# Kernel tuning notes

Measured on AMD Instinct MI355X. Metric: run time of the kernel, lower is better.

## Reference

```python
import jax, jax.numpy as jnp
import numpy as np

# Model hyperparameters (Mamba(dim=256, expand=1, d_state=16, bimamba_type='v2'))
D_MODEL = 256      # dim; expand=1 -> d_inner = D_MODEL
D_STATE = 16
DT_RANK = 16       # ceil(256/16)
D_CONV = 4
BATCH = 2
SEQ = 4096         # H*W = 64*64


def _ln(x, g, b, eps=1e-5):
    m = jnp.mean(x, axis=-1, keepdims=True)
    v = jnp.mean((x - m) ** 2, axis=-1, keepdims=True)
    return (x - m) * jax.lax.rsqrt(v + eps) * g + b


def _causal_dwconv(x, w, b):
    # x: [B, L, d], w: [d, 1, K] (depthwise), causal padding K-1 on the left
    xt = jnp.transpose(x, (0, 2, 1))  # [B, d, L]
    y = jax.lax.conv_general_dilated(
        xt, w, window_strides=(1,), padding=[(w.shape[-1] - 1, 0)],
        dimension_numbers=('NCH', 'OIH', 'NCH'), feature_group_count=xt.shape[1])
    return jnp.transpose(y + b[None, :, None], (0, 2, 1))


def _selective_scan(u, dt, Bm, Cm, A, D, z):
    # u, dt, z: [B, L, d]; Bm, Cm: [B, L, N]; A: [d, N]; D: [d]
    def step(h, inp):
        dt_t, B_t, C_t, u_t = inp            # [B,d], [B,N], [B,N], [B,d]
        h = h * jnp.exp(dt_t[:, :, None] * A) + (dt_t * u_t)[:, :, None] * B_t[:, None, :]
        y = jnp.einsum('bdn,bn->bd', h, C_t)
        return h, y

    h0 = jnp.zeros((u.shape[0], u.shape[2], A.shape[1]), u.dtype)
    xs = (jnp.transpose(dt, (1, 0, 2)), jnp.transpose(Bm, (1, 0, 2)),
          jnp.transpose(Cm, (1, 0, 2)), jnp.transpose(u, (1, 0, 2)))
    _, ys = jax.lax.scan(step, h0, xs)       # ys: [L, B, d]
    y = jnp.transpose(ys, (1, 0, 2)) + u * D
    return y * jax.nn.silu(z)                # SiLU(z) gating (done inside mamba_inner_fn)


def _mamba_dir(xin, z, conv_w, conv_b, xproj_w, dtproj_w, dtproj_b, A_log, D):
    u = jax.nn.silu(_causal_dwconv(xin, conv_w, conv_b))
    dbl = u @ xproj_w.T                       # [B, L, dt_rank + 2*N]
    dt = dbl[..., :DT_RANK]
    Bm = dbl[..., DT_RANK:DT_RANK + D_STATE]
    Cm = dbl[..., DT_RANK + D_STATE:]
    dt = jax.nn.softplus(dt @ dtproj_w.T + dtproj_b)
    return _selective_scan(u, dt, Bm, Cm, -jnp.exp(A_log), D, z)


def setup_inputs() -> dict:
    key = jax.random.key(0)
    ks = jax.random.split(key, 24)
    d, N, R, K = D_MODEL, D_STATE, DT_RANK, D_CONV
    s = 0.02
    A_log = jnp.log(jnp.tile(jnp.arange(1, N + 1, dtype=jnp.float32)[None, :], (d, 1)))
    return {
        'input': jax.random.normal(ks[0], (BATCH, SEQ, d), jnp.float32),
        'norm_g': jnp.ones((d,), jnp.float32),
        'norm_b': jnp.zeros((d,), jnp.float32),
        'in_proj_w': jax.random.normal(ks[1], (2 * d, d), jnp.float32) * s,
        # forward-direction SSM params
        'conv_w': jax.random.normal(ks[2], (d, 1, K), jnp.float32) * 0.1,
        'conv_b': jnp.zeros((d,), jnp.float32),
        'xproj_w': jax.random.normal(ks[3], (R + 2 * N, d), jnp.float32) * s,
        'dtproj_w': jax.random.normal(ks[4], (d, R), jnp.float32) * 0.1,
        'dtproj_b': jax.random.normal(ks[5], (d,), jnp.float32) * 0.1 - 4.0,
        'A_log': A_log,
        'Dp': jnp.ones((d,), jnp.float32),
        # backward-direction SSM params (bimamba v2)
        'conv_w_b': jax.random.normal(ks[6], (d, 1, K), jnp.float32) * 0.1,
        'conv_b_b': jnp.zeros((d,), jnp.float32),
        'xproj_w_b': jax.random.normal(ks[7], (R + 2 * N, d), jnp.float32) * s,
        'dtproj_w_b': jax.random.normal(ks[8], (d, R), jnp.float32) * 0.1,
        'dtproj_b_b': jax.random.normal(ks[9], (d,), jnp.float32) * 0.1 - 4.0,
        'A_log_b': A_log,
        'Dp_b': jnp.ones((d,), jnp.float32),
        # pre-out_proj norm (use_norm=True) and out projection
        'out_norm_g': jnp.ones((d,), jnp.float32),
        'out_norm_b': jnp.zeros((d,), jnp.float32),
        'out_proj_w': jax.random.normal(ks[10], (d, d), jnp.float32) * s,
        'post_norm_g': jnp.ones((d,), jnp.float32),
        'post_norm_b': jnp.zeros((d,), jnp.float32),
    }


def reference(input, norm_g, norm_b, in_proj_w,
              conv_w, conv_b, xproj_w, dtproj_w, dtproj_b, A_log, Dp,
              conv_w_b, conv_b_b, xproj_w_b, dtproj_w_b, dtproj_b_b, A_log_b, Dp_b,
              out_norm_g, out_norm_b, out_proj_w, post_norm_g, post_norm_b):
    skip = input
    x = _ln(input, norm_g, norm_b)
    xz = x @ in_proj_w.T                      # [B, L, 2d]
    xin, z = jnp.split(xz, 2, axis=-1)
    # forward direction
    y_f = _mamba_dir(xin, z, conv_w, conv_b, xproj_w, dtproj_w, dtproj_b, A_log, Dp)
    # backward direction: flip sequence, run, flip back
    y_b = _mamba_dir(xin[:, ::-1], z[:, ::-1], conv_w_b, conv_b_b, xproj_w_b,
                     dtproj_w_b, dtproj_b_b, A_log_b, Dp_b)[:, ::-1]
    y = (y_f + y_b) * 0.5                     # if_devide_out=True
    y = _ln(y, out_norm_g, out_norm_b)        # use_norm=True
    out = y @ out_proj_w.T
    out = _ln(out, post_norm_g, post_norm_b)
    return out + skip
```

## Files before the change

kernel.cpp:

```cpp
#include <hip/hip_runtime.h>
#include <math.h>

#define DM 256
#define SQ 4096
#define BT 2
#define NS 16
#define NTOK (BT*SQ)
#define NCHK 128
#define CHL (SQ/NCHK)
#define LOG2E 1.4426950408889634f

typedef __attribute__((ext_vector_type(8))) short short8;
typedef __attribute__((ext_vector_type(4))) float f32x4;

__device__ __forceinline__ float sigm_(float x){ return 1.f/(1.f+__expf(-x)); }
__device__ __forceinline__ float silu_(float x){ return x*sigm_(x); }
__device__ __forceinline__ float softplus_(float x){ return (x>20.f)? x : log1pf(__expf(x)); }
__device__ __forceinline__ unsigned short f2bf(float f){
  unsigned int u = __float_as_uint(f);
  unsigned int r = (u + 0x7FFFu + ((u>>16)&1u)) >> 16;
  return (unsigned short)r;
}
__device__ __forceinline__ float bf2f(unsigned short u){
  return __uint_as_float(((unsigned int)u)<<16);
}

__global__ __launch_bounds__(256) void k_prep(
    const float* __restrict__ x, const float* __restrict__ g, const float* __restrict__ nb,
    unsigned short* __restrict__ xl,
    const float* __restrict__ Win, unsigned short* __restrict__ Wbin,
    const float* __restrict__ xw_f, const float* __restrict__ xw_b,
    const float* __restrict__ dtw_f, const float* __restrict__ dtw_b,
    unsigned short* __restrict__ Wcatb,
    const float* __restrict__ Wout, unsigned short* __restrict__ Wbout)
{
  int bx = blockIdx.x;
  int tid = threadIdx.x;
  if (bx < NTOK/4){
    int tok = bx*4 + (tid>>6);
    int lane = tid & 63;
    const float* row = x + (size_t)tok*DM;
    float4 v = *(const float4*)(row + lane*4);
    float s = v.x+v.y+v.z+v.w;
    float ss = v.x*v.x+v.y*v.y+v.z*v.z+v.w*v.w;
    #pragma unroll
    for (int o=32;o>0;o>>=1){ s += __shfl_xor(s,o,64); ss += __shfl_xor(ss,o,64); }
    float m = s*(1.f/DM);
    float r = rsqrtf(ss*(1.f/DM)-m*m+1e-5f);
    float4 gv = *(const float4*)(g + lane*4);
    float4 bv = *(const float4*)(nb + lane*4);
    ushort4 o4;
    o4.x = f2bf((v.x-m)*r*gv.x+bv.x);
    o4.y = f2bf((v.y-m)*r*gv.y+bv.y);
    o4.z = f2bf((v.z-m)*r*gv.z+bv.z);
    o4.w = f2bf((v.w-m)*r*gv.w+bv.w);
    *(ushort4*)(xl + (size_t)tok*DM + lane*4) = o4;
  } else if (bx < NTOK/4 + 128){
    int i = ((bx - NTOK/4)*256 + tid)*4;
    float4 v = *(const float4*)(Win + i);
    ushort4 o4; o4.x=f2bf(v.x); o4.y=f2bf(v.y); o4.z=f2bf(v.z); o4.w=f2bf(v.w);
    *(ushort4*)(Wbin + i) = o4;
  } else if (bx < NTOK/4 + 136){
    int idx = bx - (NTOK/4 + 128);
    int dir = idx >> 2;
    int kc = (idx & 3)*64;
    const float* xw  = dir? xw_b : xw_f;
    const float* dtw = dir? dtw_b : dtw_f;
    int d = tid;
    float dw[16];
    #pragma unroll
    for (int r=0;r<16;r++) dw[r] = dtw[d*16+r];
    unsigned short* Wd = Wcatb + (size_t)dir*320*DM + (size_t)d*DM + kc;
    for (int kk=0;kk<64;kk++){
      float acc = 0.f;
      #pragma unroll
      for (int r=0;r<16;r++) acc += dw[r]*xw[r*DM + kc + kk];
      Wd[kk] = f2bf(acc);
    }
    if (d < 64){
      unsigned short* Wr = Wcatb + (size_t)dir*320*DM + (size_t)(256+d)*DM + kc;
      if (d < 32){
        const float* src = xw + (size_t)(16+d)*DM + kc;
        for (int kk=0;kk<64;kk++) Wr[kk] = f2bf(src[kk]);
      } else {
        for (int kk=0;kk<64;kk++) Wr[kk] = 0;
      }
    }
  } else {
    int i = ((bx - (NTOK/4 + 136))*256 + tid)*4;
    float4 v = *(const float4*)(Wout + i);
    ushort4 o4; o4.x=f2bf(v.x); o4.y=f2bf(v.y); o4.z=f2bf(v.z); o4.w=f2bf(v.w);
    *(ushort4*)(Wbout + i) = o4;
  }
}

__global__ __launch_bounds__(256) void k_inproj_conv(
    const unsigned short* __restrict__ xl, const unsigned short* __restrict__ Wb,
    const float* __restrict__ cw_f, const float* __restrict__ cb_f,
    const float* __restrict__ cw_b, const float* __restrict__ cb_b,
    unsigned short* __restrict__ ufb, unsigned short* __restrict__ ubb,
    unsigned short* __restrict__ zb)
{
  __shared__ float xs[134][68];
  __shared__ unsigned short xh[6][256];
  int tid = threadIdx.x;
  int wid = tid >> 6, lane = tid & 63;
  int wm = wid >> 1, wn = wid & 1;
  int row0 = blockIdx.x*128 + wm*64;
  int col0 = blockIdx.y*64 + wn*32;
  int lr = lane & 15, lg = lane >> 4;
  f32x4 acc[4][2];
  #pragma unroll
  for (int m=0;m<4;m++)
    #pragma unroll
    for (int n=0;n<2;n++) acc[m][n] = (f32x4){0.f,0.f,0.f,0.f};

  #pragma unroll
  for (int k0=0;k0<DM;k0+=32){
    short8 a[4], b[2];
    #pragma unroll
    for (int m=0;m<4;m++)
      a[m] = *(const short8*)(xl + (size_t)(row0 + m*16 + lr)*DM + k0 + lg*8);
    #pragma unroll
    for (int n=0;n<2;n++)
      b[n] = *(const short8*)(Wb + (size_t)(col0 + n*16 + lr)*DM + k0 + lg*8);
    #pragma unroll
    for (int m=0;m<4;m++)
      #pragma unroll
      for (int n=0;n<2;n++)
        acc[m][n] = __builtin_amdgcn_mfma_f32_16x16x32_bf16(a[m], b[n], acc[m][n], 0,0,0);
  }
  if (blockIdx.y >= 4){
    int cb = col0 - 256;
    #pragma unroll
    for (int m=0;m<4;m++)
      #pragma unroll
      for (int n=0;n<2;n++)
        #pragma unroll
        for (int r=0;r<4;r++){
          int rr = row0 + m*16 + lg*4 + r;
          int cc = cb + n*16 + lr;
          zb[(size_t)rr*DM + cc] = f2bf(acc[m][n][r]);
        }
    return;
  }
  #pragma unroll
  for (int m=0;m<4;m++)
    #pragma unroll
    for (int n=0;n<2;n++)
      #pragma unroll
      for (int r=0;r<4;r++)
        xs[wm*64 + m*16 + lg*4 + r + 3][wn*32 + n*16 + lr] = acc[m][n][r];
  int b_  = blockIdx.x >> 5;
  int lt0 = (blockIdx.x & 31)*128;
  for (int i=tid; i<6*256; i+=256){
    int hr = i >> 8, k = i & 255;
    int lt = (hr<3)? (lt0-3+hr) : (lt0+128+(hr-3));
    unsigned short v = 0;
    if (lt >= 0 && lt < SQ) v = xl[((size_t)b_*SQ+lt)*DM + k];
    xh[hr][k] = v;
  }
  __syncthreads();
  for (int i=tid; i<384; i+=256){
    int hr = i >> 6, col = i & 63;
    int gcol = blockIdx.y*64 + col;
    float acch = 0.f;
    for (int k=0;k<256;k+=8){
      short8 xa = *(const short8*)&xh[hr][k];
      short8 wv = *(const short8*)(Wb + (size_t)gcol*DM + k);
      #pragma unroll
      for (int e=0;e<8;e++) acch += bf2f((unsigned short)xa[e])*bf2f((unsigned short)wv[e]);
    }
    int xr = (hr<3)? hr : (131 + hr - 3);
    xs[xr][col] = acch;
  }
  __syncthreads();
  int col = tid & 63, tg = tid >> 6;
  int gd = blockIdx.y*64 + col;
  float wf0=cw_f[gd*4], wf1=cw_f[gd*4+1], wf2=cw_f[gd*4+2], wf3=cw_f[gd*4+3];
  float wb0=cw_b[gd*4], wb1=cw_b[gd*4+1], wb2=cw_b[gd*4+2], wb3=cw_b[gd*4+3];
  float bfv = cb_f[gd], bbv = cb_b[gd];
  for (int i=0;i<32;i++){
    int r = tg*32 + i;
    float x0=xs[r][col], x1=xs[r+1][col], x2=xs[r+2][col], x3=xs[r+3][col];
    float vf = silu_(bfv + wf0*x0 + wf1*x1 + wf2*x2 + wf3*x3);
    ufb[((size_t)b_*SQ + lt0 + r)*DM + gd] = f2bf(vf);
    float x4=xs[r+4][col], x5=xs[r+5][col], x6=xs[r+6][col];
    float vb = silu_(bbv + wb3*x3 + wb2*x4 + wb1*x5 + wb0*x6);
    ubb[((size_t)b_*SQ + (SQ-1-(lt0+r)))*DM + gd] = f2bf(vb);
  }
}

__global__ __launch_bounds__(256) void k_xproj_mfma(
    const unsigned short* __restrict__ ufb, const unsigned short* __restrict__ ubb,
    const unsigned short* __restrict__ Wcatb,
    const float* __restrict__ dtbias_f, const float* __restrict__ dtbias_b,
    unsigned short* __restrict__ dt16f, unsigned short* __restrict__ dt16b,
    float* __restrict__ bmf, float* __restrict__ cmf,
    float* __restrict__ bmb, float* __restrict__ cmb)
{
  int dir = blockIdx.z;
  const unsigned short* u  = dir? ubb : ufb;
  const unsigned short* Wc = Wcatb + (size_t)dir*320*DM;
  const float* dbi = dir? dtbias_b : dtbias_f;
  unsigned short* dt = dir? dt16b : dt16f;
  float* bm = dir? bmb : bmf;
  float* cm = dir? cmb : cmf;
  int tid = threadIdx.x;
  int wid = tid >> 6, lane = tid & 63;
  int wm = wid >> 1, wn = wid & 1;
  int row0 = blockIdx.x*128 + wm*64;
  int col0 = blockIdx.y*64 + wn*32;
  int lr = lane & 15, lg = lane >> 4;
  f32x4 acc[4][2];
  #pragma unroll
  for (int m=0;m<4;m++)
    #pragma unroll
    for (int n=0;n<2;n++) acc[m][n] = (f32x4){0.f,0.f,0.f,0.f};
  #pragma unroll
  for (int k0=0;k0<DM;k0+=32){
    short8 a[4], b[2];
    #pragma unroll
    for (int m=0;m<4;m++)
      a[m] = *(const short8*)(u + (size_t)(row0 + m*16 + lr)*DM + k0 + lg*8);
    #pragma unroll
    for (int n=0;n<2;n++)
      b[n] = *(const short8*)(Wc + (size_t)(col0 + n*16 + lr)*DM + k0 + lg*8);
    #pragma unroll
    for (int m=0;m<4;m++)
      #pragma unroll
      for (int n=0;n<2;n++)
        acc[m][n] = __builtin_amdgcn_mfma_f32_16x16x32_bf16(a[m], b[n], acc[m][n], 0,0,0);
  }
  if (blockIdx.y < 4){
    #pragma unroll
    for (int n=0;n<2;n++){
      int cc = col0 + n*16 + lr;
      float bias = dbi[cc];
      #pragma unroll
      for (int m=0;m<4;m++)
        #pragma unroll
        for (int r=0;r<4;r++){
          int rr = row0 + m*16 + lg*4 + r;
          dt[(size_t)rr*DM + cc] = f2bf(softplus_(acc[m][n][r] + bias));
        }
    }
  } else if (wn == 0){
    #pragma unroll
    for (int n=0;n<2;n++){
      float* outp = n ? cm : bm;
      #pragma unroll
      for (int m=0;m<4;m++)
        #pragma unroll
        for (int r=0;r<4;r++){
          int rr = row0 + m*16 + lg*4 + r;
          outp[(size_t)rr*NS + lr] = acc[m][n][r];
        }
    }
  }
}

__global__ __launch_bounds__(256) void k_scan1(
    const unsigned short* __restrict__ dtf, const unsigned short* __restrict__ dtb,
    const unsigned short* __restrict__ ufb, const unsigned short* __restrict__ ubb,
    const float* __restrict__ bmf, const float* __restrict__ bmb,
    const float* __restrict__ alog_f, const float* __restrict__ alog_b,
    float* __restrict__ dtsf, float* __restrict__ hsf,
    float* __restrict__ dtsb, float* __restrict__ hsb)
{
  int c = blockIdx.x, b = blockIdx.y, dir = blockIdx.z;
  const unsigned short* dt = dir? dtb : dtf;
  const unsigned short* u  = dir? ubb : ufb;
  const float* bmp= dir? bmb : bmf;
  const float* al = dir? alog_b : alog_f;
  float* dts_out = dir? dtsb : dtsf;
  float* hs = dir? hsb : hsf;
  int d = threadIdx.x;
  __shared__ float sB[CHL*NS];
  for (int i=threadIdx.x;i<CHL*NS;i+=256) sB[i] = bmp[((size_t)b*SQ + c*CHL)*NS + i];
  float A2[NS];
  #pragma unroll
  for (int n=0;n<NS;n++) A2[n] = -__expf(al[d*NS+n])*LOG2E;
  float h[NS] = {};
  float dts = 0.f;
  __syncthreads();
  size_t idx = ((size_t)b*SQ + c*CHL)*DM + d;
  unsigned short dtr = dt[idx], ur = u[idx];
  for (int t=0;t<CHL;t++){
    unsigned short dtn=0, un=0;
    if (t+1 < CHL){ dtn = dt[idx+DM]; un = u[idx+DM]; }
    float dtv = bf2f(dtr);
    float uv  = bf2f(ur);
    float du  = dtv*uv;
    dts += dtv;
    #pragma unroll
    for (int n=0;n<NS;n++) h[n] = h[n]*exp2f(dtv*A2[n]) + du*sB[t*NS+n];
    dtr = dtn; ur = un; idx += DM;
  }
  size_t o = (((size_t)b*NCHK + c)*DM + d)*NS;
  #pragma unroll
  for (int n=0;n<NS;n++) hs[o+n] = h[n];
  dts_out[((size_t)b*NCHK + c)*DM + d] = dts;
}

__global__ __launch_bounds__(256) void k_scan2(
    const float* __restrict__ dtsf, float* __restrict__ hsf,
    const float* __restrict__ dtsb, float* __restrict__ hsb,
    const float* __restrict__ alog_f, const float* __restrict__ alog_b)
{
  __shared__ float segA[8][32], segV[8][32];
  int b = blockIdx.y, dir = blockIdx.z;
  const float* dts = dir? dtsb : dtsf;
  float* hs = dir? hsb : hsf;
  const float* al = dir? alog_b : alog_f;
  int tid = threadIdx.x;
  int chain = blockIdx.x*32 + (tid & 31);
  int seg = tid >> 5;
  int dch = chain >> 4;
  float A2 = -__expf(al[chain])*LOG2E;
  size_t base = (size_t)b*NCHK*4096 + chain;
  size_t dbase = (size_t)b*NCHK*DM + dch;
  float Ac = 1.f, Vc = 0.f;
  for (int i=0;i<16;i++){
    int c = seg*16 + i;
    float a = exp2f(A2*dts[dbase + (size_t)c*DM]);
    float v = hs[base + (size_t)c*4096];
    Vc = a*Vc + v;
    Ac = Ac*a;
  }
  segA[seg][tid&31] = Ac; segV[seg][tid&31] = Vc;
  __syncthreads();
  float pre = 0.f;
  for (int s=0;s<seg;s++) pre = segA[s][tid&31]*pre + segV[s][tid&31];
  float xv = pre;
  for (int i=0;i<16;i++){
    int c = seg*16 + i;
    size_t idx = base + (size_t)c*4096;
    float a = exp2f(A2*dts[dbase + (size_t)c*DM]);
    float v = hs[idx];
    hs[idx] = xv;
    xv = a*xv + v;
  }
}

__global__ __launch_bounds__(256) void k_scan3(
    const unsigned short* __restrict__ dtf, const unsigned short* __restrict__ dtb,
    const unsigned short* __restrict__ ufb, const unsigned short* __restrict__ ubb,
    const float* __restrict__ bmf, const float* __restrict__ bmb,
    const float* __restrict__ cmf, const float* __restrict__ cmb,
    const float* __restrict__ alf, const float* __restrict__ alb,
    const float* __restrict__ Df, const float* __restrict__ Db,
    const unsigned short* __restrict__ zb,
    const float* __restrict__ hsf, const float* __restrict__ hsb,
    unsigned short* __restrict__ yf, unsigned short* __restrict__ yb)
{
  int c = blockIdx.x, b = blockIdx.y;
  int dir = blockIdx.z;
  const unsigned short* dt = dir? dtb : dtf;
  const unsigned short* u  = dir? ubb : ufb;
  const float* bmp= dir? bmb : bmf;
  const float* cmp= dir? cmb : cmf;
  const float* al = dir? alb : alf;
  const float* Dv = dir? Db  : Df;
  const float* hs = dir? hsb : hsf;
  unsigned short* yout = dir? yb : yf;
  int d = threadIdx.x;
  __shared__ float sB[CHL*NS];
  __shared__ float sC[CHL*NS];
  for (int i=threadIdx.x;i<CHL*NS;i+=256){
    sB[i] = bmp[((size_t)b*SQ + c*CHL)*NS + i];
    sC[i] = cmp[((size_t)b*SQ + c*CHL)*NS + i];
  }
  float A2[NS], h[NS];
  size_t o = (((size_t)b*NCHK + c)*DM + d)*NS;
  #pragma unroll
  for (int n=0;n<NS;n++){ A2[n] = -__expf(al[d*NS+n])*LOG2E; h[n] = hs[o+n]; }
  float Dd = Dv[d];
  __syncthreads();
  int t0g = c*CHL;
  size_t idx = ((size_t)b*SQ + t0g)*DM + d;
  long zstep = dir ? -(long)DM : (long)DM;
  size_t zidx = ((size_t)b*SQ + (dir ? (SQ-1-t0g) : t0g))*DM + d;
  unsigned short dtr = dt[idx], ur = u[idx], zr = zb[zidx];
  for (int t=0;t<CHL;t++){
    unsigned short dtn=0, un=0, zn=0;
    if (t+1 < CHL){
      dtn = dt[idx+DM]; un = u[idx+DM]; zn = zb[zidx+zstep];
    }
    float dtv = bf2f(dtr);
    float uv  = bf2f(ur);
    float du  = dtv*uv;
    float y = 0.f;
    #pragma unroll
    for (int n=0;n<NS;n++){
      h[n] = h[n]*exp2f(dtv*A2[n]) + du*sB[t*NS+n];
      y += h[n]*sC[t*NS+n];
    }
    y += uv*Dd;
    float zv = bf2f(zr);
    yout[zidx] = f2bf(y * (zv * sigm_(zv)));
    dtr = dtn; ur = un; zr = zn;
    idx += DM; zidx += zstep;
  }
}

#define SOS 266
__global__ __launch_bounds__(256) void k_final2(
    const unsigned short* __restrict__ y16f, const unsigned short* __restrict__ y16b,
    const float* __restrict__ og, const float* __restrict__ ob,
    const unsigned short* __restrict__ Wb,
    const float* __restrict__ pg, const float* __restrict__ pb,
    const float* __restrict__ skip, float* __restrict__ out)
{
  __shared__ unsigned short yn[32][272];
  __shared__ float sOut[32*SOS];
  __shared__ float sm[32], sr[32];
  int tid = threadIdx.x;
  int wid = tid >> 6, lane = tid & 63;
  int row0 = blockIdx.x*32;
  for (int j=0;j<8;j++){
    int rrow = wid*8 + j;
    size_t base = (size_t)(row0+rrow)*DM + lane*4;
    ushort4 hf = *(const ushort4*)(y16f + base);
    ushort4 hb = *(const ushort4*)(y16b + base);
    float4 v;
    v.x = 0.5f*(bf2f(hf.x)+bf2f(hb.x));
    v.y = 0.5f*(bf2f(hf.y)+bf2f(hb.y));
    v.z = 0.5f*(bf2f(hf.z)+bf2f(hb.z));
    v.w = 0.5f*(bf2f(hf.w)+bf2f(hb.w));
    float s = v.x+v.y+v.z+v.w;
    float ss = v.x*v.x+v.y*v.y+v.z*v.z+v.w*v.w;
    #pragma unroll
    for (int o=32;o>0;o>>=1){ s += __shfl_xor(s,o,64); ss += __shfl_xor(ss,o,64); }
    float m = s*(1.f/DM);
    float r = rsqrtf(ss*(1.f/DM)-m*m+1e-5f);
    float4 gv = *(const float4*)(og + lane*4);
    float4 bv = *(const float4*)(ob + lane*4);
    ushort4 o4;
    o4.x = f2bf((v.x-m)*r*gv.x+bv.x);
    o4.y = f2bf((v.y-m)*r*gv.y+bv.y);
    o4.z = f2bf((v.z-m)*r*gv.z+bv.z);
    o4.w = f2bf((v.w-m)*r*gv.w+bv.w);
    *(ushort4*)&yn[rrow][lane*4] = o4;
  }
  __syncthreads();
  int lr = lane & 15, lg = lane >> 4;
  int col0 = wid*64;
  f32x4 acc[2][4];
  #pragma unroll
  for (int m=0;m<2;m++)
    #pragma unroll
    for (int n=0;n<4;n++) acc[m][n] = (f32x4){0.f,0.f,0.f,0.f};
  #pragma unroll
  for (int k0=0;k0<DM;k0+=32){
    short8 a[2], b[4];
    #pragma unroll
    for (int m=0;m<2;m++)
      a[m] = *(const short8*)&yn[m*16 + lr][k0 + lg*8];
    #pragma unroll
    for (int n=0;n<4;n++)
      b[n] = *(const short8*)(Wb + (size_t)(col0 + n*16 + lr)*DM + k0 + lg*8);
    #pragma unroll
    for (int m=0;m<2;m++)
      #pragma unroll
      for (int n=0;n<4;n++)
        acc[m][n] = __builtin_amdgcn_mfma_f32_16x16x32_bf16(a[m], b[n], acc[m][n], 0,0,0);
  }
  #pragma unroll
  for (int m=0;m<2;m++)
    #pragma unroll
    for (int n=0;n<4;n++)
      #pragma unroll
      for (int r=0;r<4;r++)
        sOut[(m*16 + lg*4 + r)*SOS + col0 + n*16 + lr] = acc[m][n][r];
  __syncthreads();
  for (int j=0;j<8;j++){
    int rrow = wid*8 + j;
    const float* rp = &sOut[rrow*SOS + lane*4];
    float2 v0 = *(const float2*)(rp);
    float2 v1 = *(const float2*)(rp+2);
    float s = v0.x+v0.y+v1.x+v1.y;
    float ss = v0.x*v0.x+v0.y*v0.y+v1.x*v1.x+v1.y*v1.y;
    #pragma unroll
    for (int o=32;o>0;o>>=1){ s += __shfl_xor(s,o,64); ss += __shfl_xor(ss,o,64); }
    if (lane==0){ float m=s*(1.f/DM); sm[rrow]=m; sr[rrow]=rsqrtf(ss*(1.f/DM)-m*m+1e-5f); }
  }
  __syncthreads();
  float gv = pg[tid], bv = pb[tid];
  for (int rrow=0;rrow<32;rrow++){
    int tok = row0 + rrow;
    float v = (sOut[rrow*SOS + tid]-sm[rrow])*sr[rrow]*gv + bv + skip[(size_t)tok*DM + tid];
    out[(size_t)tok*DM + tid] = v;
  }
}

extern "C" void kernel_launch(void* const* d_in, const int* in_sizes, int n_in,
                              void* d_out, int out_size, void* d_ws, size_t ws_size,
                              hipStream_t stream)
{
  const float* input      = (const float*)d_in[0];
  const float* norm_g     = (const float*)d_in[1];
  const float* norm_b     = (const float*)d_in[2];
  const float* in_proj_w  = (const float*)d_in[3];
  const float* conv_w     = (const float*)d_in[4];
  const float* conv_b     = (const float*)d_in[5];
  const float* xproj_w    = (const float*)d_in[6];
  const float* dtproj_w   = (const float*)d_in[7];
  const float* dtproj_b   = (const float*)d_in[8];
  const float* A_log      = (const float*)d_in[9];
  const float* Dp         = (const float*)d_in[10];
  const float* conv_w_b   = (const float*)d_in[11];
  const float* conv_b_b   = (const float*)d_in[12];
  const float* xproj_w_b  = (const float*)d_in[13];
  const float* dtproj_w_b = (const float*)d_in[14];
  const float* dtproj_b_b = (const float*)d_in[15];
  const float* A_log_b    = (const float*)d_in[16];
  const float* Dp_b       = (const float*)d_in[17];
  const float* out_norm_g = (const float*)d_in[18];
  const float* out_norm_b = (const float*)d_in[19];
  const float* out_proj_w = (const float*)d_in[20];
  const float* post_norm_g= (const float*)d_in[21];
  const float* post_norm_b= (const float*)d_in[22];
  float* out = (float*)d_out;

  float* ws = (float*)d_ws;
  const size_t M2 = (size_t)NTOK*DM;
  const size_t SCH = (size_t)BT*NCHK*DM*NS;
  unsigned short* y16f = (unsigned short*)ws;
  unsigned short* y16b = (unsigned short*)ws + M2;
  unsigned short* zbuf = (unsigned short*)(ws + M2);
  unsigned short* auxw = (unsigned short*)(ws + M2 + M2/2);
  unsigned short* Wbin  = auxw;
  unsigned short* Wcatb = auxw + 131072;
  unsigned short* Wbout = auxw + 131072 + 163840;
  unsigned short* dt16f = (unsigned short*)(ws + 3*M2);
  unsigned short* dt16b = dt16f + M2;
  unsigned short* ufb = (unsigned short*)(ws + 4*M2);
  unsigned short* ubb = ufb + M2;
  float* p   = ws + 5*M2;
  float* bmf = p;              p += (size_t)NTOK*NS;
  float* cmf = p;              p += (size_t)NTOK*NS;
  float* bmb = p;              p += (size_t)NTOK*NS;
  float* cmb = p;              p += (size_t)NTOK*NS;
  float* dtsf = p;             p += (size_t)BT*NCHK*DM;
  float* dtsb = p;             p += (size_t)BT*NCHK*DM;
  float* hsf = p;              p += SCH;
  float* hsb = p;              p += SCH;
  unsigned short* xlbf = (unsigned short*)hsf;

  k_prep<<<NTOK/4 + 136 + 64, 256, 0, stream>>>(input, norm_g, norm_b, xlbf,
                                                in_proj_w, Wbin,
                                                xproj_w, xproj_w_b, dtproj_w, dtproj_w_b, Wcatb,
                                                out_proj_w, Wbout);
  k_inproj_conv<<<dim3(NTOK/128, 8, 1), 256, 0, stream>>>(xlbf, Wbin,
                                                          conv_w, conv_b, conv_w_b, conv_b_b,
                                                          ufb, ubb, zbuf);
  k_xproj_mfma<<<dim3(NTOK/128, 5, 2), 256, 0, stream>>>(ufb, ubb, Wcatb,
                                                         dtproj_b, dtproj_b_b,
                                                         dt16f, dt16b, bmf, cmf, bmb, cmb);
  k_scan1<<<dim3(NCHK, BT, 2), 256, 0, stream>>>(dt16f, dt16b, ufb, ubb, bmf, bmb,
                                                 A_log, A_log_b, dtsf, hsf, dtsb, hsb);
  k_scan2<<<dim3(DM*NS/32, BT, 2), 256, 0, stream>>>(dtsf, hsf, dtsb, hsb, A_log, A_log_b);
  k_scan3<<<dim3(NCHK, BT, 2), 256, 0, stream>>>(dt16f, dt16b, ufb, ubb, bmf, bmb, cmf, cmb,
                                                 A_log, A_log_b, Dp, Dp_b, zbuf, hsf, hsb,
                                                 y16f, y16b);
  k_final2<<<NTOK/32, 256, 0, stream>>>(y16f, y16b, out_norm_g, out_norm_b, Wbout,
                                        post_norm_g, post_norm_b, input, out);
}
```

Measured before the change: 150.2 us.

## Double scan chunk count and drop manual prefetch in chunked scan kernels

Raises the number of sequence chunks from 128 to 256, halving chunk length, so scan1 and scan3 launch twice as many blocks with shorter serial loops. The chunk-combine kernel scan2 now walks 32 chunks per segment instead of 16, lengthening its serial pass and doubling the state data it reads and writes. The explicit register prefetch of the next timestep's dt/u/z in scan1 and scan3 is removed in favour of direct indexed loads, leaving latency hiding to the compiler and the extra occupancy.

```diff
diff --git a/kernel.cpp b/kernel.cpp
--- a/kernel.cpp
+++ b/kernel.cpp
@@ -6,7 +6,7 @@
 #define BT 2
 #define NS 16
 #define NTOK (BT*SQ)
-#define NCHK 128
+#define NCHK 256
 #define CHL (SQ/NCHK)
 #define LOG2E 1.4426950408889634f
 
@@ -284,18 +284,14 @@
   float h[NS] = {};
   float dts = 0.f;
   __syncthreads();
-  size_t idx = ((size_t)b*SQ + c*CHL)*DM + d;
-  unsigned short dtr = dt[idx], ur = u[idx];
   for (int t=0;t<CHL;t++){
-    unsigned short dtn=0, un=0;
-    if (t+1 < CHL){ dtn = dt[idx+DM]; un = u[idx+DM]; }
-    float dtv = bf2f(dtr);
-    float uv  = bf2f(ur);
+    size_t idx = ((size_t)b*SQ + c*CHL + t)*DM + d;
+    float dtv = bf2f(dt[idx]);
+    float uv  = bf2f(u[idx]);
     float du  = dtv*uv;
     dts += dtv;
     #pragma unroll
     for (int n=0;n<NS;n++) h[n] = h[n]*exp2f(dtv*A2[n]) + du*sB[t*NS+n];
-    dtr = dtn; ur = un; idx += DM;
   }
   size_t o = (((size_t)b*NCHK + c)*DM + d)*NS;
   #pragma unroll
@@ -321,8 +317,8 @@
   size_t base = (size_t)b*NCHK*4096 + chain;
   size_t dbase = (size_t)b*NCHK*DM + dch;
   float Ac = 1.f, Vc = 0.f;
-  for (int i=0;i<16;i++){
-    int c = seg*16 + i;
+  for (int i=0;i<32;i++){
+    int c = seg*32 + i;
     float a = exp2f(A2*dts[dbase + (size_t)c*DM]);
     float v = hs[base + (size_t)c*4096];
     Vc = a*Vc + v;
@@ -333,8 +329,8 @@
   float pre = 0.f;
   for (int s=0;s<seg;s++) pre = segA[s][tid&31]*pre + segV[s][tid&31];
   float xv = pre;
-  for (int i=0;i<16;i++){
-    int c = seg*16 + i;
+  for (int i=0;i<32;i++){
+    int c = seg*32 + i;
     size_t idx = base + (size_t)c*4096;
     float a = exp2f(A2*dts[dbase + (size_t)c*DM]);
     float v = hs[idx];
@@ -377,18 +373,11 @@
   for (int n=0;n<NS;n++){ A2[n] = -__expf(al[d*NS+n])*LOG2E; h[n] = hs[o+n]; }
   float Dd = Dv[d];
   __syncthreads();
-  int t0g = c*CHL;
-  size_t idx = ((size_t)b*SQ + t0g)*DM + d;
-  long zstep = dir ? -(long)DM : (long)DM;
-  size_t zidx = ((size_t)b*SQ + (dir ? (SQ-1-t0g) : t0g))*DM + d;
-  unsigned short dtr = dt[idx], ur = u[idx], zr = zb[zidx];
   for (int t=0;t<CHL;t++){
-    unsigned short dtn=0, un=0, zn=0;
-    if (t+1 < CHL){
-      dtn = dt[idx+DM]; un = u[idx+DM]; zn = zb[zidx+zstep];
-    }
-    float dtv = bf2f(dtr);
-    float uv  = bf2f(ur);
+    int gt = c*CHL + t;
+    size_t idx = ((size_t)b*SQ + gt)*DM + d;
+    float dtv = bf2f(dt[idx]);
+    float uv  = bf2f(u[idx]);
     float du  = dtv*uv;
     float y = 0.f;
     #pragma unroll
@@ -397,10 +386,10 @@
       y += h[n]*sC[t*NS+n];
     }
     y += uv*Dd;
-    float zv = bf2f(zr);
-    yout[zidx] = f2bf(y * (zv * sigm_(zv)));
-    dtr = dtn; ur = un; zr = zn;
-    idx += DM; zidx += zstep;
+    int torig = dir ? (SQ-1-gt) : gt;
+    size_t oidx = ((size_t)b*SQ + torig)*DM + d;
+    float zv = bf2f(zb[oidx]);
+    yout[oidx] = f2bf(y * (zv * sigm_(zv)));
   }
 }
 
```

After: 155.0 us. +3.2%, slower.
